# Kernel optimization log

Measured on AMD Instinct MI355X. Metric: run time of the kernel, lower is better.

The kernel has to match this reference:

```python
import jax, jax.numpy as jnp
import numpy as np

EMBED_DIM = 512
N_HEADS = 8
HEAD_DIM = EMBED_DIM // N_HEADS
N_BINS = 512
MAX_BIN = 256
SCALE = 1.0 / np.sqrt(HEAD_DIM)


def _l2norm(x):
    # manifold.project onto unit sphere along last dim
    n = jnp.sqrt(jnp.sum(x * x, axis=-1, keepdims=True))
    return x / jnp.maximum(n, 1e-12)


def setup_inputs() -> dict:
    rng = jax.random.key(0)
    ks = jax.random.split(rng, 13)
    B, N, D = 1, 2048, EMBED_DIM
    s = 1.0 / np.sqrt(D)
    cen = jax.random.normal(ks[12], (N_BINS, HEAD_DIM), dtype=jnp.float32)
    return {
        "query": jax.random.normal(ks[0], (B, N, D), dtype=jnp.float32),
        "key": jax.random.normal(ks[1], (B, N, D), dtype=jnp.float32),
        "value": jax.random.normal(ks[2], (B, N, D), dtype=jnp.float32),
        "Wq": jax.random.normal(ks[3], (D, D), dtype=jnp.float32) * s,
        "bq": jax.random.normal(ks[4], (D,), dtype=jnp.float32) * s,
        "Wk": jax.random.normal(ks[5], (D, D), dtype=jnp.float32) * s,
        "bk": jax.random.normal(ks[6], (D,), dtype=jnp.float32) * s,
        "Wv": jax.random.normal(ks[7], (D, D), dtype=jnp.float32) * s,
        "bv": jax.random.normal(ks[8], (D,), dtype=jnp.float32) * s,
        "Wo": jax.random.normal(ks[9], (D, D), dtype=jnp.float32) * s,
        "bo": jax.random.normal(ks[10], (D,), dtype=jnp.float32) * s,
        "centroids": _l2norm(cen),  # unit bin centroids of dim head_dim
    }


def reference(query, key, value, Wq, bq, Wk, bk, Wv, bv, Wo, bo, centroids):
    B, Nq, D = query.shape
    Nk = key.shape[1]
    H, hd = N_HEADS, HEAD_DIM

    def split(x):  # [B,N,D] -> [B,H,N,hd]
        return x.reshape(B, -1, H, hd).transpose(0, 2, 1, 3)

    q = split(query @ Wq.T + bq)
    k = split(key @ Wk.T + bk)
    v = split(value @ Wv.T + bv)

    # manifold.project (sphere): attention uses the projected q/k, raw v
    qn = _l2norm(q)
    kn = _l2norm(k)

    # DavisCache: nearest-centroid bin id  [B,H,N]
    qb = jnp.argmax(jnp.einsum('bhnd,cd->bhnc', qn, centroids), axis=-1).astype(jnp.int32)
    kb = jnp.argmax(jnp.einsum('bhnd,cd->bhnc', kn, centroids), axis=-1).astype(jnp.int32)

    # neighboring_bins(qb, radius=1) on a ring: kb in {qb-1, qb, qb+1} mod N_BINS
    diff = (qb[..., :, None] - kb[..., None, :]) % N_BINS  # [B,H,Nq,Nk]
    neigh = (diff <= 1) | (diff >= N_BINS - 1)

    # truncate to first MAX_BIN selected keys (index order), as in the loop
    rank = jnp.cumsum(neigh.astype(jnp.int32), axis=-1)  # inclusive count
    sel = neigh & (rank <= MAX_BIN)
    # fallback: empty neighbor set -> all keys, then truncated to first MAX_BIN
    fallback = (jnp.arange(Nk, dtype=jnp.int32) < MAX_BIN)
    mask = jnp.where(neigh.any(axis=-1, keepdims=True), sel, fallback)

    scores = jnp.einsum('bhqd,bhkd->bhqk', qn, kn) * jnp.float32(SCALE)
    scores = jnp.where(mask, scores, jnp.float32(-1e30))
    attn = jax.nn.softmax(scores, axis=-1)  # dropout=0.0 (eval)
    out = jnp.einsum('bhqk,bhkd->bhqd', attn, v)

    out = out.transpose(0, 2, 1, 3).reshape(B, Nq, D)
    return out @ Wo.T + bo
```

## Files before the change

### kernel.cpp

```cpp
#include <hip/hip_runtime.h>
#include <hip/hip_bf16.h>

#define NTOK 2048
#define EMBED 512
#define NHEADS 8
#define HD 64
#define NBINS 512
#define MAXSEL 256

typedef unsigned short u16;
typedef unsigned int u32;

__device__ __forceinline__ float lof(u32 u){ return __uint_as_float(u << 16); }
__device__ __forceinline__ float hif(u32 u){ return __uint_as_float(u & 0xffff0000u); }
__device__ __forceinline__ float bf2f(u16 u){ return __uint_as_float(((u32)u) << 16); }
__device__ __forceinline__ u16 f2b(float f){
    __hip_bfloat16 h = __float2bfloat16(f);
    return *(u16*)&h;
}
__device__ __forceinline__ u32 pack2(float lo, float hi){
    return (u32)f2b(lo) | ((u32)f2b(hi) << 16);
}
__device__ __forceinline__ void fma8(const float* x, u32 ux, u32 uy, u32 uz, u32 uw, float& a){
    a += x[0]*lof(ux) + x[1]*hif(ux) + x[2]*lof(uy) + x[3]*hif(uy)
       + x[4]*lof(uz) + x[5]*hif(uz) + x[6]*lof(uw) + x[7]*hif(uw);
}

__device__ __forceinline__ u32 sniffp(const void* p){
    const u16* s = (const u16*)p;
    float m = 0.f;
    #pragma unroll
    for (int k=0; k<64; k++) m = fmaxf(m, fabsf(bf2f(s[2*k])));
    return (m > 100.f) ? 1u : 0u;
}

__device__ __forceinline__ void ub2(const uint4& u, float4& f0, float4& f1){
    f0 = make_float4(lof(u.x), hif(u.x), lof(u.y), hif(u.y));
    f1 = make_float4(lof(u.z), hif(u.z), lof(u.w), hif(u.w));
}

__device__ __forceinline__ void fma16x2(const float* xp,
    const float4& a0, const float4& a1, const float4& a2, const float4& a3,
    const float4& b0, const float4& b1, const float4& b2, const float4& b3,
    float& A, float& B)
{
    float4 x0 = *(const float4*)(xp);
    float4 x1 = *(const float4*)(xp+4);
    float4 x2 = *(const float4*)(xp+8);
    float4 x3 = *(const float4*)(xp+12);
    A += x0.x*a0.x; A += x0.y*a0.y; A += x0.z*a0.z; A += x0.w*a0.w;
    A += x1.x*a1.x; A += x1.y*a1.y; A += x1.z*a1.z; A += x1.w*a1.w;
    A += x2.x*a2.x; A += x2.y*a2.y; A += x2.z*a2.z; A += x2.w*a2.w;
    A += x3.x*a3.x; A += x3.y*a3.y; A += x3.z*a3.z; A += x3.w*a3.w;
    B += x0.x*b0.x; B += x0.y*b0.y; B += x0.z*b0.z; B += x0.w*b0.w;
    B += x1.x*b1.x; B += x1.y*b1.y; B += x1.z*b1.z; B += x1.w*b1.w;
    B += x2.x*b2.x; B += x2.y*b2.y; B += x2.z*b2.z; B += x2.w*b2.w;
    B += x3.x*b3.x; B += x3.y*b3.y; B += x3.z*b3.z; B += x3.w*b3.w;
}

__global__ __launch_bounds__(256) void projqkv_kernel(
    const void* __restrict__ Xq, const void* __restrict__ Xk, const void* __restrict__ Xv,
    const void* __restrict__ Wq, const void* __restrict__ bq,
    const void* __restrict__ Wk, const void* __restrict__ bk,
    const void* __restrict__ Wv, const void* __restrict__ bv,
    const void* __restrict__ cen,
    void* __restrict__ outQ,
    u16* __restrict__ Kb, u16* __restrict__ Vb,
    u16* __restrict__ qbin, u16* __restrict__ kbin)
{
    int which = blockIdx.y;
    const void *X, *W, *Bb;
    if (which==0){ X=Xq; W=Wq; Bb=bq; }
    else if (which==1){ X=Xk; W=Wk; Bb=bk; }
    else { X=Xv; W=Wv; Bb=bv; }
    u32 fx = sniffp(X), fw = sniffp(W), fb = sniffp(Bb);
    int r0 = blockIdx.x * 8;
    int t = threadIdx.x;

    __shared__ __align__(16) float ubuf[4608];
    __shared__ __align__(16) float ps[64*65];
    __shared__ float nrm2[64][4];
    __shared__ float invn[64];
    __shared__ float bvl[64][8];
    __shared__ int   bil[64][8];

    float* xstage = ps;
    for (int i=t; i<1024; i+=256){
        int row = i>>7, c4 = i&127;
        float4 v;
        if (!fx){
            const u32* xp = (const u32*)((const u16*)X + (size_t)(r0+row)*EMBED);
            u32 a = xp[c4*2], b = xp[c4*2+1];
            v = make_float4(lof(a), hif(a), lof(b), hif(b));
        } else {
            v = ((const float4*)((const float*)X + (size_t)(r0+row)*EMBED))[c4];
        }
        *(float4*)(xstage + row*516 + c4*4) = v;
    }
    __syncthreads();

    float acc2[8][2];
    #pragma unroll
    for (int r=0;r<8;r++){ acc2[r][0]=0.f; acc2[r][1]=0.f; }

    if (fw){
        const float* w1 = (const float*)W + (size_t)t*EMBED;
        const float* w2 = (const float*)W + (size_t)(t+256)*EMBED;
        float4 pa0 = *(const float4*)(w1+ 0), pa1 = *(const float4*)(w1+ 4),
               pa2 = *(const float4*)(w1+ 8), pa3 = *(const float4*)(w1+12);
        float4 pb0 = *(const float4*)(w2+ 0), pb1 = *(const float4*)(w2+ 4),
               pb2 = *(const float4*)(w2+ 8), pb3 = *(const float4*)(w2+12);
        #pragma unroll 1
        for (int k0=0; k0<512; k0+=32){
            float4 qa0 = *(const float4*)(w1+k0+16), qa1 = *(const float4*)(w1+k0+20),
                   qa2 = *(const float4*)(w1+k0+24), qa3 = *(const float4*)(w1+k0+28);
            float4 qb0 = *(const float4*)(w2+k0+16), qb1 = *(const float4*)(w2+k0+20),
                   qb2 = *(const float4*)(w2+k0+24), qb3 = *(const float4*)(w2+k0+28);
            #pragma unroll
            for (int r=0;r<8;r++)
                fma16x2(xstage + r*516 + k0, pa0,pa1,pa2,pa3, pb0,pb1,pb2,pb3,
                        acc2[r][0], acc2[r][1]);
            if (k0+32 < 512){
                pa0 = *(const float4*)(w1+k0+32); pa1 = *(const float4*)(w1+k0+36);
                pa2 = *(const float4*)(w1+k0+40); pa3 = *(const float4*)(w1+k0+44);
                pb0 = *(const float4*)(w2+k0+32); pb1 = *(const float4*)(w2+k0+36);
                pb2 = *(const float4*)(w2+k0+40); pb3 = *(const float4*)(w2+k0+44);
            }
            #pragma unroll
            for (int r=0;r<8;r++)
                fma16x2(xstage + r*516 + k0+16, qa0,qa1,qa2,qa3, qb0,qb1,qb2,qb3,
                        acc2[r][0], acc2[r][1]);
        }
    } else {
        const uint4* w1 = (const uint4*)((const u16*)W + (size_t)t*EMBED);
        const uint4* w2 = (const uint4*)((const u16*)W + (size_t)(t+256)*EMBED);
        uint4 pa0 = w1[0], pa1 = w1[1], pb0 = w2[0], pb1 = w2[1];
        #pragma unroll 1
        for (int k0=0; k0<512; k0+=32){
            int u = k0>>3;
            uint4 qa0 = w1[u+2], qa1 = w1[u+3], qb0 = w2[u+2], qb1 = w2[u+3];
            float4 a0,a1,a2,a3,b0,b1,b2,b3;
            ub2(pa0,a0,a1); ub2(pa1,a2,a3); ub2(pb0,b0,b1); ub2(pb1,b2,b3);
            #pragma unroll
            for (int r=0;r<8;r++)
                fma16x2(xstage + r*516 + k0, a0,a1,a2,a3, b0,b1,b2,b3,
                        acc2[r][0], acc2[r][1]);
            if (k0+32 < 512){ pa0 = w1[u+4]; pa1 = w1[u+5]; pb0 = w2[u+4]; pb1 = w2[u+5]; }
            ub2(qa0,a0,a1); ub2(qa1,a2,a3); ub2(qb0,b0,b1); ub2(qb1,b2,b3);
            #pragma unroll
            for (int r=0;r<8;r++)
                fma16x2(xstage + r*516 + k0+16, a0,a1,a2,a3, b0,b1,b2,b3,
                        acc2[r][0], acc2[r][1]);
        }
    }
    __syncthreads();
    {
        float b0 = fb ? ((const float*)Bb)[t]     : bf2f(((const u16*)Bb)[t]);
        float b1 = fb ? ((const float*)Bb)[t+256] : bf2f(((const u16*)Bb)[t+256]);
        int h0 = t>>6, c0 = t&63, h1 = (t+256)>>6, c1 = (t+256)&63;
        #pragma unroll
        for (int r=0;r<8;r++){
            ps[(r*8+h0)*65 + c0] = acc2[r][0]+b0;
            ps[(r*8+h1)*65 + c1] = acc2[r][1]+b1;
        }
    }
    __syncthreads();

    if (which == 2){
        int hr = t>>2, q4 = t&3;
        int row = hr>>3, head = hr&7;
        const float* src = ps + hr*65 + q4*16;
        u16* dst = Vb + (size_t)(r0+row)*EMBED + head*64 + q4*16;
        #pragma unroll
        for (int j8=0;j8<2;j8++){
            uint4 v;
            v.x = pack2(src[j8*8+0],src[j8*8+1]); v.y = pack2(src[j8*8+2],src[j8*8+3]);
            v.z = pack2(src[j8*8+4],src[j8*8+5]); v.w = pack2(src[j8*8+6],src[j8*8+7]);
            ((uint4*)dst)[j8] = v;
        }
        return;
    }

    u32 fc = sniffp(cen);
    int rg = t>>3, cg = t&7;
    float best[2] = {-3.4e38f,-3.4e38f};
    int   bidx[2] = {0,0};
    float cpre[16];
    #pragma unroll
    for (int it=0; it<16; it++){
        int e = t + it*256, j = e>>6, k = e&63;
        cpre[it] = fc ? ((const float*)cen)[(size_t)j*HD + k]
                      : bf2f(((const u16*)cen)[(size_t)j*HD + k]);
    }
    for (int tt=0; tt<8; tt++){
        __syncthreads();
        #pragma unroll
        for (int it=0; it<16; it++){
            int e = t + it*256, j = e>>6, k = e&63;
            ubuf[k*68 + j] = cpre[it];
        }
        if (tt < 7){
            #pragma unroll
            for (int it=0; it<16; it++){
                int e = t + it*256, j = e>>6, k = e&63;
                int gj = (tt+1)*64 + j;
                cpre[it] = fc ? ((const float*)cen)[(size_t)gj*HD + k]
                              : bf2f(((const u16*)cen)[(size_t)gj*HD + k]);
            }
        }
        __syncthreads();
        float acc[2][8];
        #pragma unroll
        for (int j=0;j<2;j++)
            #pragma unroll
            for (int c=0;c<8;c++) acc[j][c]=0.f;
        const float* pr0 = ps + (2*rg)*65;
        const float* pr1 = pr0 + 65;
        for (int k=0;k<64;k++){
            float a0 = pr0[k], a1 = pr1[k];
            const float4* cp = (const float4*)(ubuf + k*68 + cg*8);
            float4 c0 = cp[0], c1 = cp[1];
            acc[0][0]+=a0*c0.x; acc[0][1]+=a0*c0.y; acc[0][2]+=a0*c0.z; acc[0][3]+=a0*c0.w;
            acc[0][4]+=a0*c1.x; acc[0][5]+=a0*c1.y; acc[0][6]+=a0*c1.z; acc[0][7]+=a0*c1.w;
            acc[1][0]+=a1*c0.x; acc[1][1]+=a1*c0.y; acc[1][2]+=a1*c0.z; acc[1][3]+=a1*c0.w;
            acc[1][4]+=a1*c1.x; acc[1][5]+=a1*c1.y; acc[1][6]+=a1*c1.z; acc[1][7]+=a1*c1.w;
        }
        #pragma unroll
        for (int j=0;j<2;j++){
            #pragma unroll
            for (int c=0;c<8;c++){
                int gi = tt*64 + cg*8 + c;
                if (acc[j][c] > best[j]){ best[j]=acc[j][c]; bidx[j]=gi; }
            }
        }
    }
    bvl[2*rg  ][cg]=best[0]; bil[2*rg  ][cg]=bidx[0];
    bvl[2*rg+1][cg]=best[1]; bil[2*rg+1][cg]=bidx[1];
    {
        int hr = t>>2, q4 = t&3;
        const float* src = ps + hr*65 + q4*16;
        float ss=0.f;
        #pragma unroll
        for (int d=0;d<16;d++) ss += src[d]*src[d];
        nrm2[hr][q4]=ss;
    }
    __syncthreads();
    if (t < 64){
        int hr = t;
        invn[hr] = 1.f / fmaxf(sqrtf(nrm2[hr][0]+nrm2[hr][1]+nrm2[hr][2]+nrm2[hr][3]), 1e-12f);
        float bv = bvl[hr][0]; int bi = bil[hr][0];
        #pragma unroll
        for (int g=1; g<8; g++){
            float ov = bvl[hr][g]; int oi = bil[hr][g];
            if (ov > bv || (ov == bv && oi < bi)){ bv = ov; bi = oi; }
        }
        u16* bins = (which==0) ? qbin : kbin;
        int token = r0 + (hr>>3), head = hr&7;
        bins[head*NTOK + token] = (u16)bi;
    }
    __syncthreads();
    {
        int hr = t>>2, q4 = t&3;
        float inv = invn[hr];
        const float* src = ps + hr*65 + q4*16;
        int row = hr>>3, head = hr&7;
        size_t off = (size_t)(r0+row)*EMBED + head*64 + q4*16;
        if (which == 1){
            u16* dst = Kb + off;
            #pragma unroll
            for (int j8=0;j8<2;j8++){
                uint4 v;
                v.x = pack2(src[j8*8+0]*inv, src[j8*8+1]*inv);
                v.y = pack2(src[j8*8+2]*inv, src[j8*8+3]*inv);
                v.z = pack2(src[j8*8+4]*inv, src[j8*8+5]*inv);
                v.w = pack2(src[j8*8+6]*inv, src[j8*8+7]*inv);
                ((uint4*)dst)[j8] = v;
            }
        } else if (!fx){
            u16* dst = (u16*)outQ + off;
            #pragma unroll
            for (int j8=0;j8<2;j8++){
                uint4 v;
                v.x = pack2(src[j8*8+0]*inv, src[j8*8+1]*inv);
                v.y = pack2(src[j8*8+2]*inv, src[j8*8+3]*inv);
                v.z = pack2(src[j8*8+4]*inv, src[j8*8+5]*inv);
                v.w = pack2(src[j8*8+6]*inv, src[j8*8+7]*inv);
                ((uint4*)dst)[j8] = v;
            }
        } else {
            float* dst = (float*)outQ + off;
            #pragma unroll
            for (int j4=0;j4<4;j4++){
                float4 v = make_float4(src[j4*4+0]*inv, src[j4*4+1]*inv,
                                       src[j4*4+2]*inv, src[j4*4+3]*inv);
                ((float4*)dst)[j4] = v;
            }
        }
    }
}

__global__ __launch_bounds__(256) void attn_kernel(
    const void* __restrict__ query,
    const u16* __restrict__ Kb, const u16* __restrict__ Vb,
    const u16* __restrict__ qbin, const u16* __restrict__ kbin,
    void* __restrict__ out)
{
    u32 fq = sniffp(query);
    int q = blockIdx.x, t = threadIdx.x;
    int wave = t>>6, lane = t&63;
    __shared__ float qs[512];
    __shared__ float sc[4][256];
    __shared__ u16   sel[4][256];

    if (!fq){
        u32 u = ((const u32*)out)[(size_t)q*256 + t];
        qs[2*t] = lof(u); qs[2*t+1] = hif(u);
    } else {
        float2 f = ((const float2*)out)[(size_t)q*256 + t];
        qs[2*t] = f.x; qs[2*t+1] = f.y;
    }
    __syncthreads();

    for (int hh=0; hh<2; hh++){
        int h = wave*2 + hh;
        int myqb = qbin[h*NTOK + q];
        const uint4* kbp = (const uint4*)(kbin + h*NTOK + lane*32);
        u32 fl = 0;
        #pragma unroll
        for (int w4=0; w4<4; w4++){
            uint4 kw = kbp[w4];
            u32 arr[4] = {kw.x, kw.y, kw.z, kw.w};
            #pragma unroll
            for (int e=0;e<4;e++){
                int b0 = (int)(arr[e] & 0xffff), b1 = (int)(arr[e] >> 16);
                int d0 = (myqb - b0) & (NBINS-1), d1 = (myqb - b1) & (NBINS-1);
                if (d0 <= 1 || d0 >= NBINS-1) fl |= 1u << (w4*8 + e*2);
                if (d1 <= 1 || d1 >= NBINS-1) fl |= 1u << (w4*8 + e*2 + 1);
            }
        }
        int cnt = __popc(fl);
        int sum = cnt;
        #pragma unroll
        for (int off=1; off<64; off<<=1){
            int v = __shfl_up(sum, off, 64);
            if (lane >= off) sum += v;
        }
        int total = __shfl(sum, 63, 64);
        int r = sum - cnt;
        if (total){
            u32 f2 = fl;
            while (f2){
                int j = __ffs(f2) - 1; f2 &= f2 - 1;
                if (r < MAXSEL) sel[wave][r] = (u16)(lane*32 + j);
                r++;
            }
        } else {
            #pragma unroll
            for (int kq=0;kq<4;kq++) sel[wave][lane*4+kq] = (u16)(lane*4+kq);
        }
        int L = total ? min(total, MAXSEL) : MAXSEL;
        __syncthreads();
        const float* qh = qs + h*64;
        float mloc = -3.4e38f;
        for (int jj=lane; jj<L; jj+=64){
            int kkey = sel[wave][jj];
            const uint4* kr = (const uint4*)(Kb + (size_t)kkey*EMBED + h*64);
            float acc = 0.f;
            #pragma unroll
            for (int p=0;p<8;p++){ uint4 u = kr[p]; fma8(qh+p*8, u.x,u.y,u.z,u.w, acc); }
            float s = acc * 0.125f;
            sc[wave][jj] = s;
            mloc = fmaxf(mloc, s);
        }
        #pragma unroll
        for (int off=32; off; off>>=1) mloc = fmaxf(mloc, __shfl_xor(mloc, off, 64));
        float ssum = 0.f;
        for (int jj=lane; jj<L; jj+=64){
            float e = __expf(sc[wave][jj] - mloc);
            sc[wave][jj] = e; ssum += e;
        }
        #pragma unroll
        for (int off=32; off; off>>=1) ssum += __shfl_xor(ssum, off, 64);
        float inv = 1.f / fmaxf(ssum, 1e-37f);
        __syncthreads();
        float acc = 0.f;
        for (int j=0; j<L; j++){
            int kkey = sel[wave][j];
            acc += sc[wave][j] * bf2f(Vb[(size_t)kkey*EMBED + h*64 + lane]);
        }
        float o = acc * inv;
        if (!fq) ((u16*)out)[(size_t)q*EMBED + h*64 + lane] = f2b(o);
        else     ((float*)out)[(size_t)q*EMBED + h*64 + lane] = o;
        __syncthreads();
    }
}

__global__ __launch_bounds__(256) void oproj_kernel(
    void* __restrict__ out, const void* __restrict__ Wo, const void* __restrict__ bo)
{
    u32 fq = sniffp(out);
    u32 fw = sniffp(Wo), fb = sniffp(bo);
    int r0 = blockIdx.x * 4;
    int t = threadIdx.x;
    __shared__ __align__(16) float xst[4*516];

    for (int i=t; i<512; i+=256){
        int row = i>>7, c4 = i&127;
        float4 v;
        if (!fq){
            const u32* xp = (const u32*)((const u16*)out + (size_t)(r0+row)*EMBED);
            u32 a = xp[c4*2], b = xp[c4*2+1];
            v = make_float4(lof(a), hif(a), lof(b), hif(b));
        } else {
            v = ((const float4*)((const float*)out + (size_t)(r0+row)*EMBED))[c4];
        }
        *(float4*)(xst + row*516 + c4*4) = v;
    }
    __syncthreads();

    float acc2[4][2];
    #pragma unroll
    for (int r=0;r<4;r++){ acc2[r][0]=0.f; acc2[r][1]=0.f; }

    if (fw){
        const float* w1 = (const float*)Wo + (size_t)t*EMBED;
        const float* w2 = (const float*)Wo + (size_t)(t+256)*EMBED;
        float4 pa0 = *(const float4*)(w1+ 0), pa1 = *(const float4*)(w1+ 4),
               pa2 = *(const float4*)(w1+ 8), pa3 = *(const float4*)(w1+12);
        float4 pb0 = *(const float4*)(w2+ 0), pb1 = *(const float4*)(w2+ 4),
               pb2 = *(const float4*)(w2+ 8), pb3 = *(const float4*)(w2+12);
        #pragma unroll 1
        for (int k0=0; k0<512; k0+=32){
            float4 qa0 = *(const float4*)(w1+k0+16), qa1 = *(const float4*)(w1+k0+20),
                   qa2 = *(const float4*)(w1+k0+24), qa3 = *(const float4*)(w1+k0+28);
            float4 qb0 = *(const float4*)(w2+k0+16), qb1 = *(const float4*)(w2+k0+20),
                   qb2 = *(const float4*)(w2+k0+24), qb3 = *(const float4*)(w2+k0+28);
            #pragma unroll
            for (int r=0;r<4;r++)
                fma16x2(xst + r*516 + k0, pa0,pa1,pa2,pa3, pb0,pb1,pb2,pb3,
                        acc2[r][0], acc2[r][1]);
            if (k0+32 < 512){
                pa0 = *(const float4*)(w1+k0+32); pa1 = *(const float4*)(w1+k0+36);
                pa2 = *(const float4*)(w1+k0+40); pa3 = *(const float4*)(w1+k0+44);
                pb0 = *(const float4*)(w2+k0+32); pb1 = *(const float4*)(w2+k0+36);
                pb2 = *(const float4*)(w2+k0+40); pb3 = *(const float4*)(w2+k0+44);
            }
            #pragma unroll
            for (int r=0;r<4;r++)
                fma16x2(xst + r*516 + k0+16, qa0,qa1,qa2,qa3, qb0,qb1,qb2,qb3,
                        acc2[r][0], acc2[r][1]);
        }
    } else {
        const uint4* w1 = (const uint4*)((const u16*)Wo + (size_t)t*EMBED);
        const uint4* w2 = (const uint4*)((const u16*)Wo + (size_t)(t+256)*EMBED);
        uint4 pa0 = w1[0], pa1 = w1[1], pb0 = w2[0], pb1 = w2[1];
        #pragma unroll 1
        for (int k0=0; k0<512; k0+=32){
            int u = k0>>3;
            uint4 qa0 = w1[u+2], qa1 = w1[u+3], qb0 = w2[u+2], qb1 = w2[u+3];
            float4 a0,a1,a2,a3,b0,b1,b2,b3;
            ub2(pa0,a0,a1); ub2(pa1,a2,a3); ub2(pb0,b0,b1); ub2(pb1,b2,b3);
            #pragma unroll
            for (int r=0;r<4;r++)
                fma16x2(xst + r*516 + k0, a0,a1,a2,a3, b0,b1,b2,b3,
                        acc2[r][0], acc2[r][1]);
            if (k0+32 < 512){ pa0 = w1[u+4]; pa1 = w1[u+5]; pb0 = w2[u+4]; pb1 = w2[u+5]; }
            ub2(qa0,a0,a1); ub2(qa1,a2,a3); ub2(qb0,b0,b1); ub2(qb1,b2,b3);
            #pragma unroll
            for (int r=0;r<4;r++)
                fma16x2(xst + r*516 + k0+16, a0,a1,a2,a3, b0,b1,b2,b3,
                        acc2[r][0], acc2[r][1]);
        }
    }
    float b0 = fb ? ((const float*)bo)[t]     : bf2f(((const u16*)bo)[t]);
    float b1 = fb ? ((const float*)bo)[t+256] : bf2f(((const u16*)bo)[t+256]);
    if (!fq){
        u16* o = (u16*)out;
        #pragma unroll
        for (int r=0;r<4;r++){
            o[(size_t)(r0+r)*EMBED + t]       = f2b(acc2[r][0]+b0);
            o[(size_t)(r0+r)*EMBED + t + 256] = f2b(acc2[r][1]+b1);
        }
    } else {
        float* o = (float*)out;
        #pragma unroll
        for (int r=0;r<4;r++){
            o[(size_t)(r0+r)*EMBED + t]       = acc2[r][0]+b0;
            o[(size_t)(r0+r)*EMBED + t + 256] = acc2[r][1]+b1;
        }
    }
}

extern "C" void kernel_launch(void* const* d_in, const int* in_sizes, int n_in,
                              void* d_out, int out_size, void* d_ws, size_t ws_size,
                              hipStream_t stream)
{
    const void* query = d_in[0];
    const void* key   = d_in[1];
    const void* value = d_in[2];
    const void* Wq = d_in[3];
    const void* bq = d_in[4];
    const void* Wk = d_in[5];
    const void* bk = d_in[6];
    const void* Wv = d_in[7];
    const void* bv = d_in[8];
    const void* Wo = d_in[9];
    const void* bo = d_in[10];
    const void* cen = d_in[11];

    char* ws = (char*)d_ws;
    u16* qbin = (u16*)ws;
    u16* kbin = (u16*)(ws + 32768);
    u16* Kb   = (u16*)(ws + 65536);
    u16* Vb   = (u16*)(ws + 65536 + (size_t)2*1024*1024);

    projqkv_kernel<<<dim3(256,3), 256, 0, stream>>>(query,key,value,Wq,bq,Wk,bk,Wv,bv,cen,
                                                    d_out,Kb,Vb,qbin,kbin);
    attn_kernel<<<2048, 256, 0, stream>>>(query,Kb,Vb,qbin,kbin,d_out);
    oproj_kernel<<<512, 256, 0, stream>>>(d_out,Wo,bo);
}
```

Baseline: 307.9 us.

## Read activations directly from global memory instead of staging in LDS; widen oproj blocks

The QKV and output projection kernels stop staging the 8-row (or 4-row) activation tile in shared memory. Every thread now reads the same activation values straight from global memory, which should broadcast through cache, and this removes one barrier. The oproj kernel moves to 512 threads with one output column each and 8 rows per block, and the centroid-scan loop is unrolled by 4 with a padded 68-float row stride for vector reads. The risks are more redundant global/L1 traffic per thread and a possible in-place hazard in oproj: it reads and writes `out`, and the added barrier only orders threads within a block, so other blocks writing disjoint rows should be fine.

```diff
diff --git a/kernel.cpp b/kernel.cpp
--- a/kernel.cpp
+++ b/kernel.cpp
@@ -39,15 +39,25 @@
     f1 = make_float4(lof(u.z), hif(u.z), lof(u.w), hif(u.w));
 }
 
-__device__ __forceinline__ void fma16x2(const float* xp,
+__device__ __forceinline__ void ldx4u(const void* X, u32 fx, int row, int k0,
+                                      float4& x0, float4& x1, float4& x2, float4& x3){
+    if (fx){
+        const float* p = (const float*)X + (size_t)row*EMBED + k0;
+        x0 = *(const float4*)(p);   x1 = *(const float4*)(p+4);
+        x2 = *(const float4*)(p+8); x3 = *(const float4*)(p+12);
+    } else {
+        const uint4* p = (const uint4*)((const u16*)X + (size_t)row*EMBED + k0);
+        uint4 u0 = p[0], u1 = p[1];
+        ub2(u0, x0, x1); ub2(u1, x2, x3);
+    }
+}
+
+__device__ __forceinline__ void fma16x2v(
+    const float4& x0, const float4& x1, const float4& x2, const float4& x3,
     const float4& a0, const float4& a1, const float4& a2, const float4& a3,
     const float4& b0, const float4& b1, const float4& b2, const float4& b3,
     float& A, float& B)
 {
-    float4 x0 = *(const float4*)(xp);
-    float4 x1 = *(const float4*)(xp+4);
-    float4 x2 = *(const float4*)(xp+8);
-    float4 x3 = *(const float4*)(xp+12);
     A += x0.x*a0.x; A += x0.y*a0.y; A += x0.z*a0.z; A += x0.w*a0.w;
     A += x1.x*a1.x; A += x1.y*a1.y; A += x1.z*a1.z; A += x1.w*a1.w;
     A += x2.x*a2.x; A += x2.y*a2.y; A += x2.z*a2.z; A += x2.w*a2.w;
@@ -56,6 +66,17 @@
     B += x1.x*b1.x; B += x1.y*b1.y; B += x1.z*b1.z; B += x1.w*b1.w;
     B += x2.x*b2.x; B += x2.y*b2.y; B += x2.z*b2.z; B += x2.w*b2.w;
     B += x3.x*b3.x; B += x3.y*b3.y; B += x3.z*b3.z; B += x3.w*b3.w;
+}
+
+__device__ __forceinline__ void fma16x1v(
+    const float4& x0, const float4& x1, const float4& x2, const float4& x3,
+    const float4& a0, const float4& a1, const float4& a2, const float4& a3,
+    float& A)
+{
+    A += x0.x*a0.x; A += x0.y*a0.y; A += x0.z*a0.z; A += x0.w*a0.w;
+    A += x1.x*a1.x; A += x1.y*a1.y; A += x1.z*a1.z; A += x1.w*a1.w;
+    A += x2.x*a2.x; A += x2.y*a2.y; A += x2.z*a2.z; A += x2.w*a2.w;
+    A += x3.x*a3.x; A += x3.y*a3.y; A += x3.z*a3.z; A += x3.w*a3.w;
 }
 
 __global__ __launch_bounds__(256) void projqkv_kernel(
@@ -78,26 +99,11 @@
     int t = threadIdx.x;
 
     __shared__ __align__(16) float ubuf[4608];
-    __shared__ __align__(16) float ps[64*65];
+    __shared__ __align__(16) float ps[64*68];
     __shared__ float nrm2[64][4];
     __shared__ float invn[64];
     __shared__ float bvl[64][8];
     __shared__ int   bil[64][8];
-
-    float* xstage = ps;
-    for (int i=t; i<1024; i+=256){
-        int row = i>>7, c4 = i&127;
-        float4 v;
-        if (!fx){
-            const u32* xp = (const u32*)((const u16*)X + (size_t)(r0+row)*EMBED);
-            u32 a = xp[c4*2], b = xp[c4*2+1];
-            v = make_float4(lof(a), hif(a), lof(b), hif(b));
-        } else {
-            v = ((const float4*)((const float*)X + (size_t)(r0+row)*EMBED))[c4];
-        }
-        *(float4*)(xstage + row*516 + c4*4) = v;
-    }
-    __syncthreads();
 
     float acc2[8][2];
     #pragma unroll
@@ -117,9 +123,12 @@
             float4 qb0 = *(const float4*)(w2+k0+16), qb1 = *(const float4*)(w2+k0+20),
                    qb2 = *(const float4*)(w2+k0+24), qb3 = *(const float4*)(w2+k0+28);
             #pragma unroll
-            for (int r=0;r<8;r++)
-                fma16x2(xstage + r*516 + k0, pa0,pa1,pa2,pa3, pb0,pb1,pb2,pb3,
-                        acc2[r][0], acc2[r][1]);
+            for (int r=0;r<8;r++){
+                float4 x0,x1,x2,x3;
+                ldx4u(X, fx, r0+r, k0, x0,x1,x2,x3);
+                fma16x2v(x0,x1,x2,x3, pa0,pa1,pa2,pa3, pb0,pb1,pb2,pb3,
+                         acc2[r][0], acc2[r][1]);
+            }
             if (k0+32 < 512){
                 pa0 = *(const float4*)(w1+k0+32); pa1 = *(const float4*)(w1+k0+36);
                 pa2 = *(const float4*)(w1+k0+40); pa3 = *(const float4*)(w1+k0+44);
@@ -127,9 +136,12 @@
                 pb2 = *(const float4*)(w2+k0+40); pb3 = *(const float4*)(w2+k0+44);
             }
             #pragma unroll
-            for (int r=0;r<8;r++)
-                fma16x2(xstage + r*516 + k0+16, qa0,qa1,qa2,qa3, qb0,qb1,qb2,qb3,
-                        acc2[r][0], acc2[r][1]);
+            for (int r=0;r<8;r++){
+                float4 x0,x1,x2,x3;
+                ldx4u(X, fx, r0+r, k0+16, x0,x1,x2,x3);
+                fma16x2v(x0,x1,x2,x3, qa0,qa1,qa2,qa3, qb0,qb1,qb2,qb3,
+                         acc2[r][0], acc2[r][1]);
+            }
         }
     } else {
         const uint4* w1 = (const uint4*)((const u16*)W + (size_t)t*EMBED);
@@ -142,26 +154,31 @@
             float4 a0,a1,a2,a3,b0,b1,b2,b3;
             ub2(pa0,a0,a1); ub2(pa1,a2,a3); ub2(pb0,b0,b1); ub2(pb1,b2,b3);
             #pragma unroll
-            for (int r=0;r<8;r++)
-                fma16x2(xstage + r*516 + k0, a0,a1,a2,a3, b0,b1,b2,b3,
-                        acc2[r][0], acc2[r][1]);
+            for (int r=0;r<8;r++){
+                float4 x0,x1,x2,x3;
+                ldx4u(X, fx, r0+r, k0, x0,x1,x2,x3);
+                fma16x2v(x0,x1,x2,x3, a0,a1,a2,a3, b0,b1,b2,b3,
+                         acc2[r][0], acc2[r][1]);
+            }
             if (k0+32 < 512){ pa0 = w1[u+4]; pa1 = w1[u+5]; pb0 = w2[u+4]; pb1 = w2[u+5]; }
             ub2(qa0,a0,a1); ub2(qa1,a2,a3); ub2(qb0,b0,b1); ub2(qb1,b2,b3);
             #pragma unroll
-            for (int r=0;r<8;r++)
-                fma16x2(xstage + r*516 + k0+16, a0,a1,a2,a3, b0,b1,b2,b3,
-                        acc2[r][0], acc2[r][1]);
-        }
-    }
-    __syncthreads();
+            for (int r=0;r<8;r++){
+                float4 x0,x1,x2,x3;
+                ldx4u(X, fx, r0+r, k0+16, x0,x1,x2,x3);
+                fma16x2v(x0,x1,x2,x3, a0,a1,a2,a3, b0,b1,b2,b3,
+                         acc2[r][0], acc2[r][1]);
+            }
+        }
+    }
     {
         float b0 = fb ? ((const float*)Bb)[t]     : bf2f(((const u16*)Bb)[t]);
         float b1 = fb ? ((const float*)Bb)[t+256] : bf2f(((const u16*)Bb)[t+256]);
         int h0 = t>>6, c0 = t&63, h1 = (t+256)>>6, c1 = (t+256)&63;
         #pragma unroll
         for (int r=0;r<8;r++){
-            ps[(r*8+h0)*65 + c0] = acc2[r][0]+b0;
-            ps[(r*8+h1)*65 + c1] = acc2[r][1]+b1;
+            ps[(r*8+h0)*68 + c0] = acc2[r][0]+b0;
+            ps[(r*8+h1)*68 + c1] = acc2[r][1]+b1;
         }
     }
     __syncthreads();
@@ -169,7 +186,7 @@
     if (which == 2){
         int hr = t>>2, q4 = t&3;
         int row = hr>>3, head = hr&7;
-        const float* src = ps + hr*65 + q4*16;
+        const float* src = ps + hr*68 + q4*16;
         u16* dst = Vb + (size_t)(r0+row)*EMBED + head*64 + q4*16;
         #pragma unroll
         for (int j8=0;j8<2;j8++){
@@ -211,19 +228,29 @@
         __syncthreads();
         float acc[2][8];
         #pragma unroll
-        for (int j=0;j<2;j++)
+        for (int j=0;j<2;j++){
             #pragma unroll
             for (int c=0;c<8;c++) acc[j][c]=0.f;
-        const float* pr0 = ps + (2*rg)*65;
-        const float* pr1 = pr0 + 65;
-        for (int k=0;k<64;k++){
-            float a0 = pr0[k], a1 = pr1[k];
-            const float4* cp = (const float4*)(ubuf + k*68 + cg*8);
-            float4 c0 = cp[0], c1 = cp[1];
-            acc[0][0]+=a0*c0.x; acc[0][1]+=a0*c0.y; acc[0][2]+=a0*c0.z; acc[0][3]+=a0*c0.w;
-            acc[0][4]+=a0*c1.x; acc[0][5]+=a0*c1.y; acc[0][6]+=a0*c1.z; acc[0][7]+=a0*c1.w;
-            acc[1][0]+=a1*c0.x; acc[1][1]+=a1*c0.y; acc[1][2]+=a1*c0.z; acc[1][3]+=a1*c0.w;
-            acc[1][4]+=a1*c1.x; acc[1][5]+=a1*c1.y; acc[1][6]+=a1*c1.z; acc[1][7]+=a1*c1.w;
+        }
+        const float* pr0 = ps + (2*rg)*68;
+        const float* pr1 = pr0 + 68;
+        #pragma unroll 1
+        for (int k4=0;k4<64;k4+=4){
+            float4 ra = *(const float4*)(pr0 + k4);
+            float4 rb = *(const float4*)(pr1 + k4);
+            const float* cbase = ubuf + k4*68 + cg*8;
+            #define SCANK(OFF, AX, BX) { \
+                const float4* cp = (const float4*)(cbase + (OFF)); \
+                float4 c0 = cp[0], c1 = cp[1]; \
+                acc[0][0]+=(AX)*c0.x; acc[0][1]+=(AX)*c0.y; acc[0][2]+=(AX)*c0.z; acc[0][3]+=(AX)*c0.w; \
+                acc[0][4]+=(AX)*c1.x; acc[0][5]+=(AX)*c1.y; acc[0][6]+=(AX)*c1.z; acc[0][7]+=(AX)*c1.w; \
+                acc[1][0]+=(BX)*c0.x; acc[1][1]+=(BX)*c0.y; acc[1][2]+=(BX)*c0.z; acc[1][3]+=(BX)*c0.w; \
+                acc[1][4]+=(BX)*c1.x; acc[1][5]+=(BX)*c1.y; acc[1][6]+=(BX)*c1.z; acc[1][7]+=(BX)*c1.w; }
+            SCANK(0,   ra.x, rb.x)
+            SCANK(68,  ra.y, rb.y)
+            SCANK(136, ra.z, rb.z)
+            SCANK(204, ra.w, rb.w)
+            #undef SCANK
         }
         #pragma unroll
         for (int j=0;j<2;j++){
@@ -238,7 +265,7 @@
     bvl[2*rg+1][cg]=best[1]; bil[2*rg+1][cg]=bidx[1];
     {
         int hr = t>>2, q4 = t&3;
-        const float* src = ps + hr*65 + q4*16;
+        const float* src = ps + hr*68 + q4*16;
         float ss=0.f;
         #pragma unroll
         for (int d=0;d<16;d++) ss += src[d]*src[d];
@@ -262,7 +289,7 @@
     {
         int hr = t>>2, q4 = t&3;
         float inv = invn[hr];
-        const float* src = ps + hr*65 + q4*16;
+        const float* src = ps + hr*68 + q4*16;
         int row = hr>>3, head = hr&7;
         size_t off = (size_t)(r0+row)*EMBED + head*64 + q4*16;
         if (which == 1){
@@ -395,99 +422,80 @@
     }
 }
 
-__global__ __launch_bounds__(256) void oproj_kernel(
+__global__ __launch_bounds__(512) void oproj_kernel(
     void* __restrict__ out, const void* __restrict__ Wo, const void* __restrict__ bo)
 {
     u32 fq = sniffp(out);
     u32 fw = sniffp(Wo), fb = sniffp(bo);
-    int r0 = blockIdx.x * 4;
+    int r0 = blockIdx.x * 8;
     int t = threadIdx.x;
-    __shared__ __align__(16) float xst[4*516];
-
-    for (int i=t; i<512; i+=256){
-        int row = i>>7, c4 = i&127;
-        float4 v;
-        if (!fq){
-            const u32* xp = (const u32*)((const u16*)out + (size_t)(r0+row)*EMBED);
-            u32 a = xp[c4*2], b = xp[c4*2+1];
-            v = make_float4(lof(a), hif(a), lof(b), hif(b));
-        } else {
-            v = ((const float4*)((const float*)out + (size_t)(r0+row)*EMBED))[c4];
-        }
-        *(float4*)(xst + row*516 + c4*4) = v;
-    }
-    __syncthreads();
-
-    float acc2[4][2];
+
+    float acc[8];
     #pragma unroll
-    for (int r=0;r<4;r++){ acc2[r][0]=0.f; acc2[r][1]=0.f; }
+    for (int r=0;r<8;r++) acc[r]=0.f;
 
     if (fw){
         const float* w1 = (const float*)Wo + (size_t)t*EMBED;
-        const float* w2 = (const float*)Wo + (size_t)(t+256)*EMBED;
         float4 pa0 = *(const float4*)(w1+ 0), pa1 = *(const float4*)(w1+ 4),
                pa2 = *(const float4*)(w1+ 8), pa3 = *(const float4*)(w1+12);
-        float4 pb0 = *(const float4*)(w2+ 0), pb1 = *(const float4*)(w2+ 4),
-               pb2 = *(const float4*)(w2+ 8), pb3 = *(const float4*)(w2+12);
         #pragma unroll 1
         for (int k0=0; k0<512; k0+=32){
             float4 qa0 = *(const float4*)(w1+k0+16), qa1 = *(const float4*)(w1+k0+20),
                    qa2 = *(const float4*)(w1+k0+24), qa3 = *(const float4*)(w1+k0+28);
-            float4 qb0 = *(const float4*)(w2+k0+16), qb1 = *(const float4*)(w2+k0+20),
-                   qb2 = *(const float4*)(w2+k0+24), qb3 = *(const float4*)(w2+k0+28);
-            #pragma unroll
-            for (int r=0;r<4;r++)
-                fma16x2(xst + r*516 + k0, pa0,pa1,pa2,pa3, pb0,pb1,pb2,pb3,
-                        acc2[r][0], acc2[r][1]);
+            #pragma unroll
+            for (int r=0;r<8;r++){
+                float4 x0,x1,x2,x3;
+                ldx4u(out, fq, r0+r, k0, x0,x1,x2,x3);
+                fma16x1v(x0,x1,x2,x3, pa0,pa1,pa2,pa3, acc[r]);
+            }
             if (k0+32 < 512){
                 pa0 = *(const float4*)(w1+k0+32); pa1 = *(const float4*)(w1+k0+36);
                 pa2 = *(const float4*)(w1+k0+40); pa3 = *(const float4*)(w1+k0+44);
-                pb0 = *(const float4*)(w2+k0+32); pb1 = *(const float4*)(w2+k0+36);
-                pb2 = *(const float4*)(w2+k0+40); pb3 = *(const float4*)(w2+k0+44);
-            }
-            #pragma unroll
-            for (int r=0;r<4;r++)
-                fma16x2(xst + r*516 + k0+16, qa0,qa1,qa2,qa3, qb0,qb1,qb2,qb3,
-                        acc2[r][0], acc2[r][1]);
+            }
+            #pragma unroll
+            for (int r=0;r<8;r++){
+                float4 x0,x1,x2,x3;
+                ldx4u(out, fq, r0+r, k0+16, x0,x1,x2,x3);
+                fma16x1v(x0,x1,x2,x3, qa0,qa1,qa2,qa3, acc[r]);
+            }
         }
     } else {
         const uint4* w1 = (const uint4*)((const u16*)Wo + (size_t)t*EMBED);
-        const uint4* w2 = (const uint4*)((const u16*)Wo + (size_t)(t+256)*EMBED);
-        uint4 pa0 = w1[0], pa1 = w1[1], pb0 = w2[0], pb1 = w2[1];
+        uint4 pa0 = w1[0], pa1 = w1[1];
         #pragma unroll 1
         for (int k0=0; k0<512; k0+=32){
             int u = k0>>3;
-            uint4 qa0 = w1[u+2], qa1 = w1[u+3], qb0 = w2[u+2], qb1 = w2[u+3];
-            float4 a0,a1,a2,a3,b0,b1,b2,b3;
-            ub2(pa0,a0,a1); ub2(pa1,a2,a3); ub2(pb0,b0,b1); ub2(pb1,b2,b3);
-            #pragma unroll
-            for (int r=0;r<4;r++)
-                fma16x2(xst + r*516 + k0, a0,a1,a2,a3, b0,b1,b2,b3,
-                        acc2[r][0], acc2[r][1]);
-            if (k0+32 < 512){ pa0 = w1[u+4]; pa1 = w1[u+5]; pb0 = w2[u+4]; pb1 = w2[u+5]; }
-            ub2(qa0,a0,a1); ub2(qa1,a2,a3); ub2(qb0,b0,b1); ub2(qb1,b2,b3);
-            #pragma unroll
-            for (int r=0;r<4;r++)
-                fma16x2(xst + r*516 + k0+16, a0,a1,a2,a3, b0,b1,b2,b3,
-                        acc2[r][0], acc2[r][1]);
-        }
-    }
-    float b0 = fb ? ((const float*)bo)[t]     : bf2f(((const u16*)bo)[t]);
-    float b1 = fb ? ((const float*)bo)[t+256] : bf2f(((const u16*)bo)[t+256]);
+            uint4 qa0 = w1[u+2], qa1 = w1[u+3];
+            float4 a0,a1,a2,a3;
+            ub2(pa0,a0,a1); ub2(pa1,a2,a3);
+            #pragma unroll
+            for (int r=0;r<8;r++){
+                float4 x0,x1,x2,x3;
+                ldx4u(out, fq, r0+r, k0, x0,x1,x2,x3);
+                fma16x1v(x0,x1,x2,x3, a0,a1,a2,a3, acc[r]);
+            }
+            if (k0+32 < 512){ pa0 = w1[u+4]; pa1 = w1[u+5]; }
+            ub2(qa0,a0,a1); ub2(qa1,a2,a3);
+            #pragma unroll
+            for (int r=0;r<8;r++){
+                float4 x0,x1,x2,x3;
+                ldx4u(out, fq, r0+r, k0+16, x0,x1,x2,x3);
+                fma16x1v(x0,x1,x2,x3, a0,a1,a2,a3, acc[r]);
+            }
+        }
+    }
+    __syncthreads();
+    float b0 = fb ? ((const float*)bo)[t] : bf2f(((const u16*)bo)[t]);
     if (!fq){
         u16* o = (u16*)out;
         #pragma unroll
-        for (int r=0;r<4;r++){
-            o[(size_t)(r0+r)*EMBED + t]       = f2b(acc2[r][0]+b0);
-            o[(size_t)(r0+r)*EMBED + t + 256] = f2b(acc2[r][1]+b1);
-        }
+        for (int r=0;r<8;r++)
+            o[(size_t)(r0+r)*EMBED + t] = f2b(acc[r]+b0);
     } else {
         float* o = (float*)out;
         #pragma unroll
-        for (int r=0;r<4;r++){
-            o[(size_t)(r0+r)*EMBED + t]       = acc2[r][0]+b0;
-            o[(size_t)(r0+r)*EMBED + t + 256] = acc2[r][1]+b1;
-        }
+        for (int r=0;r<8;r++)
+            o[(size_t)(r0+r)*EMBED + t] = acc[r]+b0;
     }
 }
 
@@ -517,5 +525,5 @@
     projqkv_kernel<<<dim3(256,3), 256, 0, stream>>>(query,key,value,Wq,bq,Wk,bk,Wv,bv,cen,
                                                     d_out,Kb,Vb,qbin,kbin);
     attn_kernel<<<2048, 256, 0, stream>>>(query,Kb,Vb,qbin,kbin,d_out);
-    oproj_kernel<<<512, 256, 0, stream>>>(d_out,Wo,bo);
-}
+    oproj_kernel<<<256, 512, 0, stream>>>(d_out,Wo,bo);
+}
```

Measured after the change: 430.4 us. 1.4x slower.
